# Optimization experiments

Hardware: AMD Instinct MI355X
Metric: run time of the kernel (lower is better)

The kernel has to match this reference:

```python
import jax, jax.numpy as jnp
import numpy as np

B, T, D = 64, 2048, 256
HID, M = 32, 3
EPS = 1e-8


def _xavier(k, shape):
    lim = (6.0 / (shape[0] + shape[1])) ** 0.5
    return jax.random.uniform(k, shape, jnp.float32, -lim, lim)


def setup_inputs() -> dict:
    key = jax.random.key(0)
    ks = jax.random.split(key, 8)
    h = jax.random.normal(ks[0], (B, T, D), dtype=jnp.float32)
    mask = jax.random.randint(ks[1], (B, T, D), 0, 2).astype(jnp.int32)
    return dict(
        h=h, mask=mask,
        Wa1=_xavier(ks[2], (D, HID)), ba1=jnp.zeros((HID,), jnp.float32),
        Wa2=_xavier(ks[3], (HID, 1)), ba2=jnp.zeros((1,), jnp.float32),
        Wr1=_xavier(ks[4], (D, HID)), br1=jnp.zeros((HID,), jnp.float32),
        Wr2=_xavier(ks[5], (HID, HID)), br2=jnp.zeros((HID,), jnp.float32),
        Wr3=_xavier(ks[6], (HID, M)), br3=jnp.zeros((M,), jnp.float32),
        temperature=jnp.ones((1,), jnp.float32),
    )


def _enhanced_stats(x, mask):
    Bn, Tn, Dn = x.shape
    dt = x.dtype
    # --- temporal: lag-1 autocorrelation (uncentered) + linear trend slope ---
    autocorr = jnp.mean(x[:, :-1, :] * x[:, 1:, :], axis=(1, 2))[:, None]
    t = jnp.arange(Tn, dtype=dt)
    tc = t - t.mean()
    xm_t = x.mean(axis=2)  # (B,T)
    num = jnp.sum(tc * (xm_t - xm_t.mean(axis=1, keepdims=True)), axis=1, keepdims=True)
    trend = num / (jnp.sum(tc ** 2) + EPS)
    # --- frequency: dominant freq + spectral entropy of channel-mean signal ---
    power = jnp.abs(jnp.fft.rfft(xm_t, axis=1)) ** 2  # (B, T//2+1)
    dom_freq = (jnp.argmax(power, axis=1).astype(dt) / (Tn / 2))[:, None]
    pn = power / (power.sum(axis=1, keepdims=True) + EPS)
    spec_ent = -jnp.sum(pn * jnp.log(pn + EPS), axis=1, keepdims=True)
    # --- statistical: skew, kurtosis, quantiles over all (T*D) values ---
    xc = x - x.mean(axis=(1, 2), keepdims=True)
    m2 = jnp.mean(xc ** 2, axis=(1, 2))
    m3 = jnp.mean(xc ** 3, axis=(1, 2))
    m4 = jnp.mean(xc ** 4, axis=(1, 2))
    skew = m3 / (m2 ** 1.5 + EPS)
    kurt = m4 / (m2 ** 2 + EPS)
    xf = x.reshape(Bn, -1)
    q = jnp.quantile(xf, jnp.array([0.25, 0.5, 0.75], dtype=dt), axis=1)  # (3,B)
    stat = jnp.stack([skew, kurt, q[0], q[1], q[2]], axis=1)
    # --- shape: peak count, zero crossings, rate of change ---
    diff = xm_t[:, 1:] - xm_t[:, :-1]
    peak = jnp.sum((diff[:, 1:] * diff[:, :-1] < 0).astype(dt), axis=1, keepdims=True) / (Tn - 2)
    xct = xm_t - xm_t.mean(axis=1, keepdims=True)
    zc = jnp.sum((xct[:, 1:] * xct[:, :-1] < 0).astype(dt), axis=1, keepdims=True) / (Tn - 1)
    roc = jnp.mean(jnp.abs(diff), axis=1, keepdims=True)
    # --- missing-data features ---
    mf = mask.astype(dt)
    observed = mf.reshape(Bn, -1).sum(axis=1, keepdims=True)
    miss_rate = 1.0 - observed / (Tn * Dn + EPS)
    dens = mf.sum(axis=2) / (Dn + EPS)  # (B,T)
    dens_var = jnp.var(dens, axis=1, ddof=1, keepdims=True)
    tmask = mf.sum(axis=2) > 0
    first_obs = jnp.where(tmask.any(axis=1, keepdims=True),
                          jnp.argmax(tmask, axis=1, keepdims=True).astype(dt) / Tn, 0.0)
    # --- channel features: mean off-diag corr + PCA top var-explained ---
    xcm = x - x.mean(axis=1, keepdims=True)  # (B,T,D)
    gram = jnp.einsum('btd,bte->bde', xcm, xcm)  # (B,D,D) = Xc^T Xc
    cov = gram / (Tn - 1 + EPS)
    std = jnp.std(x, axis=1, ddof=1)  # (B,D)
    corr = cov / (std[:, :, None] * std[:, None, :] + EPS)
    off_diag = 1.0 - jnp.eye(Dn, dtype=dt)
    mean_corr = (jnp.sum(corr * off_diag, axis=(1, 2)) / (Dn * (Dn - 1) + EPS))[:, None]
    # singular values of Xc squared == eigenvalues of Xc^T Xc
    ev = jnp.linalg.eigvalsh(gram)  # ascending (B,D)
    var_exp = (ev[:, -1] / jnp.sum(ev, axis=1))[:, None]
    return jnp.concatenate([autocorr, trend, dom_freq, spec_ent, stat,
                            peak, zc, roc, miss_rate, dens_var, first_obs,
                            mean_corr, var_exp], axis=1)  # (B, 17)


def _direct_routing(h, Wa1, ba1, Wa2, ba2, Wr1, br1, Wr2, br2, Wr3, br3, temperature):
    attn_logits = jnp.tanh(h @ Wa1 + ba1) @ Wa2 + ba2  # (B,T,1)
    attn_w = jax.nn.softmax(attn_logits, axis=1)
    h_pooled = jnp.sum(h * attn_w, axis=1)  # (B,D)
    z = jax.nn.relu(h_pooled @ Wr1 + br1)   # dropout is identity in eval
    z = jax.nn.relu(z @ Wr2 + br2)
    logits = z @ Wr3 + br3
    temp = jnp.clip(temperature, 0.5, 2.0)
    alpha = jax.nn.softmax(logits / temp, axis=-1)
    return alpha, h_pooled


def reference(h, mask, Wa1, ba1, Wa2, ba2, Wr1, br1, Wr2, br2, Wr3, br3, temperature):
    alpha, h_pooled = _direct_routing(h, Wa1, ba1, Wa2, ba2,
                                      Wr1, br1, Wr2, br2, Wr3, br3, temperature)
    stats = _enhanced_stats(h, mask)
    return alpha, h_pooled, stats
```

## Files before the change

### kernel.cpp

```cpp
#include <hip/hip_runtime.h>
#include <math.h>
#include <stdint.h>

#define B 64
#define T 2048
#define D 256
#define HID 32
#define NSEL 6
#define NBIN 8192
#define CAP 8192
#define LCAP 2048
#define EPS 1e-8

#define A_S1 0
#define A_S2 1
#define A_S3 2
#define A_S4 3
#define A_AC 4
#define A_Y2 5
#define A_DIAG 6
#define A_TRACE 7
#define A_N 16

#define NAPPLY 32

typedef __attribute__((ext_vector_type(4))) short short4v;
typedef __attribute__((ext_vector_type(8))) short short8v;
typedef __attribute__((ext_vector_type(4))) float f32x4;

__device__ __forceinline__ unsigned int f2key(float f) {
    unsigned int u = __float_as_uint(f);
    return (u & 0x80000000u) ? ~u : (u | 0x80000000u);
}
__device__ __forceinline__ float key2f(unsigned int k) {
    unsigned int u = (k & 0x80000000u) ? (k ^ 0x80000000u) : ~k;
    return __uint_as_float(u);
}
__device__ __forceinline__ short f2bf(float f) {
    unsigned int u = __float_as_uint(f);
    unsigned int r = u + 0x7FFFu + ((u >> 16) & 1u);
    return (short)(r >> 16);
}

__global__ __launch_bounds__(256) void k_pass1(const float* __restrict__ x, const int* __restrict__ mask,
        double* __restrict__ xm, float* __restrict__ rowm,
        double* __restrict__ cs1, double* __restrict__ cs2, double* __restrict__ accum) {
    int b = blockIdx.x >> 4;
    int blk = blockIdx.x & 15;
    int wave = threadIdx.x >> 6;
    int lane = threadIdx.x & 63;
    int ts = blk * 128 + wave * 32;
    const float* xb = x + (size_t)b * T * D;
    const int* mb = mask + (size_t)b * T * D;
    double c1l[4] = {0, 0, 0, 0}, c2l[4] = {0, 0, 0, 0};
    double s1 = 0, s2 = 0, s3 = 0, s4 = 0, ac = 0;
    float pa[4] = {0, 0, 0, 0};
    for (int r = 0; r < 32; ++r) {
        int t = ts + r;
        float4 xv = *(const float4*)(xb + (size_t)t * D + lane * 4);
        int4 mv = *(const int4*)(mb + (size_t)t * D + lane * 4);
        double rs = (double)xv.x + (double)xv.y + (double)xv.z + (double)xv.w;
        int rm = mv.x + mv.y + mv.z + mv.w;
        for (int o = 32; o > 0; o >>= 1) { rs += __shfl_down(rs, o); rm += __shfl_down(rm, o); }
        if (lane == 0) {
            xm[(size_t)b * T + t] = rs * (1.0 / 256.0);
            rowm[(size_t)b * T + t] = (float)rm;
        }
        float xa[4] = {xv.x, xv.y, xv.z, xv.w};
        #pragma unroll
        for (int j = 0; j < 4; ++j) {
            double xd = (double)xa[j];
            double x2 = xd * xd;
            s1 += xd; s2 += x2; s3 += x2 * xd; s4 += x2 * x2;
            c1l[j] += xd; c2l[j] += x2;
        }
        if (r > 0) {
            #pragma unroll
            for (int j = 0; j < 4; ++j) ac += (double)pa[j] * (double)xa[j];
        }
        pa[0] = xa[0]; pa[1] = xa[1]; pa[2] = xa[2]; pa[3] = xa[3];
    }
    if (ts + 32 <= T - 1) {
        float4 xn = *(const float4*)(xb + (size_t)(ts + 32) * D + lane * 4);
        float na[4] = {xn.x, xn.y, xn.z, xn.w};
        #pragma unroll
        for (int j = 0; j < 4; ++j) ac += (double)pa[j] * (double)na[j];
    }
    for (int o = 32; o > 0; o >>= 1) {
        s1 += __shfl_down(s1, o); s2 += __shfl_down(s2, o);
        s3 += __shfl_down(s3, o); s4 += __shfl_down(s4, o);
        ac += __shfl_down(ac, o);
    }
    if (lane == 0) {
        atomicAdd(&accum[b * A_N + A_S1], s1);
        atomicAdd(&accum[b * A_N + A_S2], s2);
        atomicAdd(&accum[b * A_N + A_S3], s3);
        atomicAdd(&accum[b * A_N + A_S4], s4);
        atomicAdd(&accum[b * A_N + A_AC], ac);
    }
    #pragma unroll
    for (int j = 0; j < 4; ++j) {
        atomicAdd(&cs1[b * D + lane * 4 + j], c1l[j]);
        atomicAdd(&cs2[b * D + lane * 4 + j], c2l[j]);
    }
}

__global__ __launch_bounds__(256) void k_chan(const double* __restrict__ cs1, const double* __restrict__ cs2,
        float* __restrict__ mu, float* __restrict__ winv, double* __restrict__ accum) {
    int b = blockIdx.x, d = threadIdx.x;
    double c1 = cs1[b * D + d], c2 = cs2[b * D + d];
    double m = c1 / (double)T;
    double c2c = c2 - c1 * c1 / (double)T;
    double var = c2c / (double)(T - 1);
    mu[b * D + d] = (float)m;
    winv[b * D + d] = (float)(1.0 / sqrt(var));
    double diag = (c2c / ((double)(T - 1) + EPS)) / (var + EPS);
    __shared__ double sd[256], st[256];
    sd[d] = diag; st[d] = c2c; __syncthreads();
    for (int o = 128; o > 0; o >>= 1) {
        if (d < o) { sd[d] += sd[d + o]; st[d] += st[d + o]; }
        __syncthreads();
    }
    if (d == 0) { accum[b * A_N + A_DIAG] = sd[0]; accum[b * A_N + A_TRACE] = st[0]; }
}

__global__ __launch_bounds__(256) void k_attn(const float* __restrict__ x,
        const float* __restrict__ Wa1, const float* __restrict__ ba1,
        const float* __restrict__ Wa2, const float* __restrict__ ba2,
        float* __restrict__ logit) {
    __shared__ float tile[256][33];
    int bid = blockIdx.x;
    int b = bid >> 3, t0 = (bid & 7) * 256;
    int tid = threadIdx.x;
    const float* xb = x + (size_t)b * T * D + (size_t)t0 * D;
    float acc[HID];
    #pragma unroll
    for (int h = 0; h < HID; ++h) acc[h] = 0.f;
    for (int dc = 0; dc < 8; ++dc) {
        __syncthreads();
        #pragma unroll
        for (int i = 0; i < 32; ++i) {
            int idx = i * 256 + tid;
            int tl = idx >> 5, dd = idx & 31;
            tile[tl][dd] = xb[(size_t)tl * D + dc * 32 + dd];
        }
        __syncthreads();
        #pragma unroll
        for (int dd = 0; dd < 32; ++dd) {
            float xval = tile[tid][dd];
            const float* wrow = Wa1 + (dc * 32 + dd) * HID;
            #pragma unroll
            for (int h = 0; h < HID; ++h) acc[h] += xval * wrow[h];
        }
    }
    float lg = ba2[0];
    #pragma unroll
    for (int h = 0; h < HID; ++h) lg += tanhf(acc[h] + ba1[h]) * Wa2[h];
    logit[(size_t)b * T + t0 + tid] = lg;
}

__global__ __launch_bounds__(256) void k_smax(const float* __restrict__ logit, float* __restrict__ smz) {
    int b = blockIdx.x, tid = threadIdx.x;
    __shared__ float sm[256];
    __shared__ double sz[256];
    float mx = -1e30f;
    for (int i = tid; i < T; i += 256) mx = fmaxf(mx, logit[(size_t)b * T + i]);
    sm[tid] = mx; __syncthreads();
    for (int o = 128; o > 0; o >>= 1) { if (tid < o) sm[tid] = fmaxf(sm[tid], sm[tid + o]); __syncthreads(); }
    float m = sm[0];
    double z = 0;
    for (int i = tid; i < T; i += 256) z += (double)expf(logit[(size_t)b * T + i] - m);
    sz[tid] = z; __syncthreads();
    for (int o = 128; o > 0; o >>= 1) { if (tid < o) sz[tid] += sz[tid + o]; __syncthreads(); }
    if (tid == 0) { smz[b * 2] = m; smz[b * 2 + 1] = (float)sz[0]; }
}

__global__ __launch_bounds__(256) void k_pool(const float* __restrict__ x,
        const float* __restrict__ logit, const float* __restrict__ smz,
        const float* __restrict__ mu, const float* __restrict__ winv,
        float* __restrict__ hpool, double* __restrict__ accum) {
    int bid = blockIdx.x;
    int b = bid >> 3, t0 = (bid & 7) * 256;
    int wave = threadIdx.x >> 6, lane = threadIdx.x & 63;
    const float* xb = x + (size_t)b * T * D;
    float m = smz[b * 2], Z = smz[b * 2 + 1];
    float4 mu4 = *(const float4*)(mu + b * D + lane * 4);
    float4 w4 = *(const float4*)(winv + b * D + lane * 4);
    double p0 = 0, p1 = 0, p2 = 0, p3 = 0, yacc = 0;
    for (int r = 0; r < 64; ++r) {
        int t = t0 + wave * 64 + r;
        float4 xv = *(const float4*)(xb + (size_t)t * D + lane * 4);
        float wt = expf(logit[(size_t)b * T + t] - m) / Z;
        p0 += (double)(wt * xv.x); p1 += (double)(wt * xv.y);
        p2 += (double)(wt * xv.z); p3 += (double)(wt * xv.w);
        double y = (double)((xv.x - mu4.x) * w4.x) + (double)((xv.y - mu4.y) * w4.y)
                 + (double)((xv.z - mu4.z) * w4.z) + (double)((xv.w - mu4.w) * w4.w);
        for (int o = 32; o > 0; o >>= 1) y += __shfl_down(y, o);
        if (lane == 0) yacc += y * y;
    }
    if (lane == 0) atomicAdd(&accum[b * A_N + A_Y2], yacc);
    atomicAdd(&hpool[b * D + lane * 4 + 0], (float)p0);
    atomicAdd(&hpool[b * D + lane * 4 + 1], (float)p1);
    atomicAdd(&hpool[b * D + lane * 4 + 2], (float)p2);
    atomicAdd(&hpool[b * D + lane * 4 + 3], (float)p3);
}

__global__ void k_route(const float* __restrict__ hpool,
        const float* __restrict__ Wr1, const float* __restrict__ br1,
        const float* __restrict__ Wr2, const float* __restrict__ br2,
        const float* __restrict__ Wr3, const float* __restrict__ br3,
        const float* __restrict__ temperature, float* __restrict__ alpha) {
    int b = blockIdx.x, tid = threadIdx.x;
    __shared__ float z1[HID], z2[HID], hp[D];
    for (int i = tid; i < D; i += 64) hp[i] = hpool[b * D + i];
    __syncthreads();
    if (tid < HID) {
        float a = br1[tid];
        for (int d = 0; d < D; ++d) a += hp[d] * Wr1[d * HID + tid];
        z1[tid] = fmaxf(a, 0.f);
    }
    __syncthreads();
    if (tid < HID) {
        float a = br2[tid];
        for (int j = 0; j < HID; ++j) a += z1[j] * Wr2[j * HID + tid];
        z2[tid] = fmaxf(a, 0.f);
    }
    __syncthreads();
    if (tid == 0) {
        float tmp = temperature[0];
        tmp = fminf(fmaxf(tmp, 0.5f), 2.0f);
        float lg[3];
        for (int k = 0; k < 3; ++k) {
            float a = br3[k];
            for (int j = 0; j < HID; ++j) a += z2[j] * Wr3[j * 3 + k];
            lg[k] = a / tmp;
        }
        float mx = fmaxf(lg[0], fmaxf(lg[1], lg[2]));
        float e0 = expf(lg[0] - mx), e1 = expf(lg[1] - mx), e2 = expf(lg[2] - mx);
        float s = e0 + e1 + e2;
        alpha[b * 3 + 0] = e0 / s; alpha[b * 3 + 1] = e1 / s; alpha[b * 3 + 2] = e2 / s;
    }
}

__global__ __launch_bounds__(256) void k_xmstats(const double* __restrict__ xm,
        const float* __restrict__ rowm, const double* __restrict__ accum,
        float* __restrict__ stats) {
    int b = blockIdx.x, tid = threadIdx.x;
    __shared__ double xs[T];
    __shared__ double r0[256], r1[256], r2[256];
    __shared__ int i0[256], i1[256];
    const double* xmb = xm + (size_t)b * T;
    for (int i = tid; i < T; i += 256) xs[i] = xmb[i];
    __syncthreads();
    double ls = 0;
    for (int i = tid; i < T; i += 256) ls += xs[i];
    r0[tid] = ls; __syncthreads();
    for (int o = 128; o > 0; o >>= 1) { if (tid < o) r0[tid] += r0[tid + o]; __syncthreads(); }
    double xmean = r0[0] / (double)T;
    __syncthreads();
    double tn = 0, roc = 0; int pk = 0, zc = 0;
    for (int i = tid; i < T; i += 256) {
        tn += ((double)i - 1023.5) * (xs[i] - xmean);
        if (i <= T - 2) {
            double d1 = xs[i + 1] - xs[i];
            roc += fabs(d1);
            if (i >= 1) { double d0 = xs[i] - xs[i - 1]; if (d0 * d1 < 0.0) pk++; }
            if ((xs[i] - xmean) * (xs[i + 1] - xmean) < 0.0) zc++;
        }
    }
    r0[tid] = tn; r1[tid] = roc; i0[tid] = pk; i1[tid] = zc; __syncthreads();
    for (int o = 128; o > 0; o >>= 1) {
        if (tid < o) { r0[tid] += r0[tid + o]; r1[tid] += r1[tid + o]; i0[tid] += i0[tid + o]; i1[tid] += i1[tid + o]; }
        __syncthreads();
    }
    double trendnum = r0[0], rocsum = r1[0];
    int pks = i0[0], zcs = i1[0];
    __syncthreads();
    double ds = 0, ds2 = 0, obs = 0; int ft = T;
    for (int i = tid; i < T; i += 256) {
        double rm = (double)rowm[(size_t)b * T + i];
        obs += rm;
        double dn = rm / (256.0 + EPS);
        ds += dn; ds2 += dn * dn;
        if (rm > 0.0 && i < ft) ft = i;
    }
    r0[tid] = ds; r1[tid] = ds2; r2[tid] = obs; i0[tid] = ft; __syncthreads();
    for (int o = 128; o > 0; o >>= 1) {
        if (tid < o) { r0[tid] += r0[tid + o]; r1[tid] += r1[tid + o]; r2[tid] += r2[tid + o]; i0[tid] = min(i0[tid], i0[tid + o]); }
        __syncthreads();
    }
    if (tid == 0) {
        double dsum = r0[0], dsq = r1[0], obst = r2[0]; int ftt = i0[0];
        const double n = (double)T * (double)D;
        const double* ab = accum + b * A_N;
        double s1 = ab[A_S1], s2 = ab[A_S2], s3 = ab[A_S3], s4 = ab[A_S4];
        double acv = ab[A_AC], y2 = ab[A_Y2], dg = ab[A_DIAG];
        double mu_ = s1 / n;
        double m2 = s2 / n - mu_ * mu_;
        double m3 = s3 / n - 3.0 * mu_ * (s2 / n) + 2.0 * mu_ * mu_ * mu_;
        double m4 = s4 / n - 4.0 * mu_ * (s3 / n) + 6.0 * mu_ * mu_ * (s2 / n) - 3.0 * mu_ * mu_ * mu_ * mu_;
        float* st = stats + b * 17;
        st[0] = (float)(acv / ((double)(T - 1) * (double)D));
        st[1] = (float)(trendnum / (715827712.0 + EPS));
        st[4] = (float)(m3 / (sqrt(m2) * m2 + EPS));
        st[5] = (float)(m4 / (m2 * m2 + EPS));
        st[9] = (float)((double)pks / (double)(T - 2));
        st[10] = (float)((double)zcs / (double)(T - 1));
        st[11] = (float)(rocsum / (double)(T - 1));
        st[12] = (float)(1.0 - obst / ((double)T * (double)D + EPS));
        double dmean = dsum / (double)T;
        st[13] = (float)((dsq - dsum * dmean) / (double)(T - 1));
        st[14] = (ftt < T) ? (float)((double)ftt / (double)T) : 0.0f;
        st[15] = (float)((y2 / ((double)(T - 1) + EPS) - dg) / ((double)D * (D - 1) + EPS));
    }
}

__global__ __launch_bounds__(256) void k_dft(const double* __restrict__ xm, double* __restrict__ power) {
    __shared__ double xs[T];
    int b = blockIdx.x / 5, kc = blockIdx.x % 5;
    int tid = threadIdx.x;
    for (int i = tid; i < T; i += 256) xs[i] = xm[(size_t)b * T + i];
    __syncthreads();
    int k = kc * 256 + tid;
    if (k <= T / 2) {
        double theta = -6.283185307179586476925286766559 * (double)k / (double)T;
        double c4 = cos(4.0 * theta), s4 = sin(4.0 * theta);
        double cr = 1.0, ci = 0.0;
        double a0r = 0, a0i = 0, a1r = 0, a1i = 0, a2r = 0, a2i = 0, a3r = 0, a3i = 0;
        #pragma unroll 4
        for (int p = 0; p < T / 4; ++p) {
            double x0 = xs[4 * p + 0], x1 = xs[4 * p + 1];
            double x2 = xs[4 * p + 2], x3 = xs[4 * p + 3];
            a0r += x0 * cr; a0i += x0 * ci;
            a1r += x1 * cr; a1i += x1 * ci;
            a2r += x2 * cr; a2i += x2 * ci;
            a3r += x3 * cr; a3i += x3 * ci;
            double ncr = cr * c4 - ci * s4;
            double nci = cr * s4 + ci * c4;
            cr = ncr; ci = nci;
        }
        double c1 = cos(theta), s1 = sin(theta);
        double ar = a0r, ai = a0i;
        ar += c1 * a1r - s1 * a1i; ai += c1 * a1i + s1 * a1r;
        double c2 = c1 * c1 - s1 * s1, s2 = 2.0 * c1 * s1;
        ar += c2 * a2r - s2 * a2i; ai += c2 * a2i + s2 * a2r;
        double c3 = c2 * c1 - s2 * s1, s3 = c2 * s1 + s2 * c1;
        ar += c3 * a3r - s3 * a3i; ai += c3 * a3i + s3 * a3r;
        power[(size_t)b * 1025 + k] = ar * ar + ai * ai;
    }
}

__global__ __launch_bounds__(256) void k_spec(const double* __restrict__ power, float* __restrict__ stats) {
    int b = blockIdx.x, tid = threadIdx.x;
    __shared__ double rv[256];
    __shared__ int ri[256];
    const double* pb = power + (size_t)b * 1025;
    double bm = -1.0; int bi = 0; double lsum = 0;
    for (int i = tid; i < 1025; i += 256) {
        double p = pb[i];
        lsum += p;
        if (p > bm) { bm = p; bi = i; }
    }
    rv[tid] = bm; ri[tid] = bi; __syncthreads();
    for (int o = 128; o > 0; o >>= 1) {
        if (tid < o) {
            if (rv[tid + o] > rv[tid] || (rv[tid + o] == rv[tid] && ri[tid + o] < ri[tid])) {
                rv[tid] = rv[tid + o]; ri[tid] = ri[tid + o];
            }
        }
        __syncthreads();
    }
    int amax = ri[0];
    __syncthreads();
    rv[tid] = lsum; __syncthreads();
    for (int o = 128; o > 0; o >>= 1) { if (tid < o) rv[tid] += rv[tid + o]; __syncthreads(); }
    double S = rv[0] + EPS;
    __syncthreads();
    double le = 0;
    for (int i = tid; i < 1025; i += 256) {
        double pn = pb[i] / S;
        le -= pn * log(pn + EPS);
    }
    rv[tid] = le; __syncthreads();
    for (int o = 128; o > 0; o >>= 1) { if (tid < o) rv[tid] += rv[tid + o]; __syncthreads(); }
    if (tid == 0) {
        stats[b * 17 + 2] = (float)((double)amax / (double)(T / 2));
        stats[b * 17 + 3] = (float)rv[0];
    }
}

__global__ __launch_bounds__(256) void k_histA(const float* __restrict__ x, unsigned int* __restrict__ hist) {
    __shared__ unsigned int lh[NBIN];
    int b = blockIdx.x >> 2, chunk = blockIdx.x & 3;
    int tid = threadIdx.x;
    for (int i = tid; i < NBIN; i += 256) lh[i] = 0;
    __syncthreads();
    const float4* xb = (const float4*)(x + (size_t)b * T * D + (size_t)chunk * (T * D / 4));
    for (int i = tid; i < T * D / 16; i += 256) {
        float4 v = xb[i];
        atomicAdd(&lh[f2key(v.x) >> 19], 1u);
        atomicAdd(&lh[f2key(v.y) >> 19], 1u);
        atomicAdd(&lh[f2key(v.z) >> 19], 1u);
        atomicAdd(&lh[f2key(v.w) >> 19], 1u);
    }
    __syncthreads();
    for (int i = tid; i < NBIN; i += 256)
        if (lh[i]) atomicAdd(&hist[(size_t)b * NBIN + i], lh[i]);
}

__global__ __launch_bounds__(256) void k_histB(const unsigned int* __restrict__ hist,
        unsigned int* __restrict__ binsel, unsigned int* __restrict__ krem) {
    int b = blockIdx.x, tid = threadIdx.x;
    __shared__ unsigned int seg[256], base[256];
    const unsigned int* hb = hist + (size_t)b * NBIN;
    unsigned int s = 0;
    for (int i = 0; i < 32; ++i) s += hb[tid * 32 + i];
    seg[tid] = s; __syncthreads();
    if (tid == 0) {
        unsigned int run = 0;
        for (int i = 0; i < 256; ++i) { base[i] = run; run += seg[i]; }
    }
    __syncthreads();
    const unsigned int targets[NSEL] = {131071u, 131072u, 262143u, 262144u, 393215u, 393216u};
    for (int q = 0; q < NSEL; ++q) {
        unsigned int k = targets[q];
        if (k >= base[tid] && k < base[tid] + seg[tid]) {
            unsigned int run = base[tid];
            for (int i = 0; i < 32; ++i) {
                unsigned int c = hb[tid * 32 + i];
                if (k < run + c) { binsel[b * NSEL + q] = tid * 32 + i; krem[b * NSEL + q] = k - run; break; }
                run += c;
            }
        }
    }
}

__global__ __launch_bounds__(256) void k_compact(const float* __restrict__ x,
        const unsigned int* __restrict__ binsel, unsigned int* __restrict__ ccnt,
        unsigned int* __restrict__ cand) {
    __shared__ unsigned int lbuf[NSEL][LCAP];
    __shared__ unsigned int lcnt[NSEL];
    __shared__ unsigned int gbase[NSEL];
    int b = blockIdx.x >> 4, chunk = blockIdx.x & 15;
    int tid = threadIdx.x;
    if (tid < NSEL) lcnt[tid] = 0;
    unsigned int bs[NSEL];
    #pragma unroll
    for (int q = 0; q < NSEL; ++q) bs[q] = binsel[b * NSEL + q];
    __syncthreads();
    const float4* xb = (const float4*)(x + (size_t)b * T * D + (size_t)chunk * (T * D / 16));
    for (int it = 0; it < 32; ++it) {
        float4 v = xb[it * 256 + tid];
        float va[4] = {v.x, v.y, v.z, v.w};
        #pragma unroll
        for (int j = 0; j < 4; ++j) {
            unsigned int u = f2key(va[j]);
            unsigned int bin = u >> 19;
            #pragma unroll
            for (int q = 0; q < NSEL; ++q) {
                if (bin == bs[q]) {
                    unsigned int p = atomicAdd(&lcnt[q], 1u);
                    if (p < LCAP) lbuf[q][p] = u;
                }
            }
        }
        __syncthreads();
        bool need = false;
        #pragma unroll
        for (int q = 0; q < NSEL; ++q) need = need || (lcnt[q] > (unsigned)(LCAP - 1024));
        if (need) {
            if (tid < NSEL) {
                unsigned int n = min(lcnt[tid], (unsigned)LCAP);
                gbase[tid] = atomicAdd(&ccnt[b * NSEL + tid], n);
            }
            __syncthreads();
            #pragma unroll
            for (int q = 0; q < NSEL; ++q) {
                unsigned int n = min(lcnt[q], (unsigned)LCAP);
                unsigned int g0 = gbase[q];
                for (unsigned int i = tid; i < n; i += 256) {
                    unsigned int p = g0 + i;
                    if (p < CAP) cand[((size_t)b * NSEL + q) * CAP + p] = lbuf[q][i];
                }
            }
            __syncthreads();
            if (tid < NSEL) lcnt[tid] = 0;
            __syncthreads();
        }
    }
    __syncthreads();
    if (tid < NSEL) {
        unsigned int n = min(lcnt[tid], (unsigned)LCAP);
        gbase[tid] = atomicAdd(&ccnt[b * NSEL + tid], n);
    }
    __syncthreads();
    #pragma unroll
    for (int q = 0; q < NSEL; ++q) {
        unsigned int n = min(lcnt[q], (unsigned)LCAP);
        unsigned int g0 = gbase[q];
        for (unsigned int i = tid; i < n; i += 256) {
            unsigned int p = g0 + i;
            if (p < CAP) cand[((size_t)b * NSEL + q) * CAP + p] = lbuf[q][i];
        }
    }
}

__global__ __launch_bounds__(256) void k_select(const unsigned int* __restrict__ cand,
        const unsigned int* __restrict__ ccnt, const unsigned int* __restrict__ binsel,
        const unsigned int* __restrict__ krem, float* __restrict__ qv) {
    int b = blockIdx.x / NSEL, q = blockIdx.x % NSEL;
    int tid = threadIdx.x;
    __shared__ unsigned int lc[CAP];
    __shared__ unsigned int rc[256];
    unsigned int n = ccnt[b * NSEL + q];
    if (n > CAP) n = CAP;
    for (unsigned int i = tid; i < n; i += 256) lc[i] = cand[((size_t)b * NSEL + q) * CAP + i];
    __syncthreads();
    unsigned int prefix = binsel[b * NSEL + q] << 19;
    unsigned int k = krem[b * NSEL + q];
    for (int bit = 18; bit >= 0; --bit) {
        unsigned int hi = prefix >> (bit + 1);
        unsigned int c = 0;
        for (unsigned int i = tid; i < n; i += 256) {
            unsigned int u = lc[i];
            if ((u >> (bit + 1)) == hi && !((u >> bit) & 1u)) c++;
        }
        rc[tid] = c; __syncthreads();
        for (int o = 128; o > 0; o >>= 1) { if (tid < o) rc[tid] += rc[tid + o]; __syncthreads(); }
        unsigned int c0 = rc[0];
        __syncthreads();
        if (k >= c0) { k -= c0; prefix |= (1u << bit); }
    }
    if (tid == 0) qv[b * NSEL + q] = key2f(prefix);
}

__global__ void k_qwrite(const float* __restrict__ qv, float* __restrict__ stats) {
    int b = threadIdx.x;
    if (b >= B) return;
    const float* qq = qv + b * NSEL;
    double q25 = 0.25 * (double)qq[0] + 0.75 * (double)qq[1];
    double q50 = 0.5 * ((double)qq[2] + (double)qq[3]);
    double q75 = 0.75 * (double)qq[4] + 0.25 * (double)qq[5];
    stats[b * 17 + 6] = (float)q25;
    stats[b * 17 + 7] = (float)q50;
    stats[b * 17 + 8] = (float)q75;
}

#define GROWS 72
__global__ __launch_bounds__(256) void k_gram(const float* __restrict__ x, const float* __restrict__ mu,
        float* __restrict__ gram) {
    __shared__ __align__(16) short lds_a[128 * GROWS];
    __shared__ __align__(16) short lds_b[128 * GROWS];
    int b = blockIdx.x >> 2;
    int ti = (blockIdx.x >> 1) & 1, tj = blockIdx.x & 1;
    int i0 = ti * 128, j0 = tj * 128;
    int tid = threadIdx.x;
    int w = tid >> 6, lane = tid & 63;
    int qd = lane >> 4, l15 = lane & 15;
    const float* xb = x + (size_t)b * T * D;
    const float* mub = mu + (size_t)b * D;
    int mc = tid & 31;
    float4 mua = *(const float4*)(mub + i0 + 4 * mc);
    float4 mub4 = *(const float4*)(mub + j0 + 4 * mc);
    f32x4 acc[2][8];
    #pragma unroll
    for (int rt = 0; rt < 2; ++rt)
        #pragma unroll
        for (int ct = 0; ct < 8; ++ct) acc[rt][ct] = (f32x4){0.f, 0.f, 0.f, 0.f};
    for (int t0 = 0; t0 < T; t0 += 64) {
        __syncthreads();
        #pragma unroll
        for (int half = 0; half < 2; ++half) {
            int mtt = (tid >> 5) + half * 8;
            int t = t0 + 4 * mtt;
            int tblk = mtt >> 1;
            int sub = (mtt & 1) * 4;
            int rot = (tblk + mc) & 7;
            {
                const float* src = xb + (size_t)t * D + i0 + 4 * mc;
                float4 r0 = *(const float4*)(src);
                float4 r1 = *(const float4*)(src + D);
                float4 r2 = *(const float4*)(src + 2 * D);
                float4 r3 = *(const float4*)(src + 3 * D);
                float a0[4] = {r0.x - mua.x, r0.y - mua.y, r0.z - mua.z, r0.w - mua.w};
                float a1[4] = {r1.x - mua.x, r1.y - mua.y, r1.z - mua.z, r1.w - mua.w};
                float a2[4] = {r2.x - mua.x, r2.y - mua.y, r2.z - mua.z, r2.w - mua.w};
                float a3[4] = {r3.x - mua.x, r3.y - mua.y, r3.z - mua.z, r3.w - mua.w};
                #pragma unroll
                for (int j = 0; j < 4; ++j) {
                    int c = 4 * mc + j;
                    short4v v4 = {f2bf(a0[j]), f2bf(a1[j]), f2bf(a2[j]), f2bf(a3[j])};
                    *(short4v*)(lds_a + c * GROWS + rot * 8 + sub) = v4;
                }
            }
            {
                const float* src = xb + (size_t)t * D + j0 + 4 * mc;
                float4 r0 = *(const float4*)(src);
                float4 r1 = *(const float4*)(src + D);
                float4 r2 = *(const float4*)(src + 2 * D);
                float4 r3 = *(const float4*)(src + 3 * D);
                float a0[4] = {r0.x - mub4.x, r0.y - mub4.y, r0.z - mub4.z, r0.w - mub4.w};
                float a1[4] = {r1.x - mub4.x, r1.y - mub4.y, r1.z - mub4.z, r1.w - mub4.w};
                float a2[4] = {r2.x - mub4.x, r2.y - mub4.y, r2.z - mub4.z, r2.w - mub4.w};
                float a3[4] = {r3.x - mub4.x, r3.y - mub4.y, r3.z - mub4.z, r3.w - mub4.w};
                #pragma unroll
                for (int j = 0; j < 4; ++j) {
                    int c = 4 * mc + j;
                    short4v v4 = {f2bf(a0[j]), f2bf(a1[j]), f2bf(a2[j]), f2bf(a3[j])};
                    *(short4v*)(lds_b + c * GROWS + rot * 8 + sub) = v4;
                }
            }
        }
        __syncthreads();
        #pragma unroll
        for (int kc = 0; kc < 2; ++kc) {
            int tblk = kc * 4 + qd;
            short8v af[2];
            #pragma unroll
            for (int rt = 0; rt < 2; ++rt) {
                int c = w * 32 + rt * 16 + l15;
                int rot = (tblk + (c >> 2)) & 7;
                af[rt] = *(const short8v*)(lds_a + c * GROWS + rot * 8);
            }
            short8v bfr[8];
            #pragma unroll
            for (int ct = 0; ct < 8; ++ct) {
                int c = ct * 16 + l15;
                int rot = (tblk + (c >> 2)) & 7;
                bfr[ct] = *(const short8v*)(lds_b + c * GROWS + rot * 8);
            }
            #pragma unroll
            for (int rt = 0; rt < 2; ++rt)
                #pragma unroll
                for (int ct = 0; ct < 8; ++ct)
                    acc[rt][ct] = __builtin_amdgcn_mfma_f32_16x16x32_bf16(af[rt], bfr[ct], acc[rt][ct], 0, 0, 0);
        }
    }
    float* gb = gram + (size_t)b * D * D;
    #pragma unroll
    for (int rt = 0; rt < 2; ++rt) {
        int rbase = i0 + w * 32 + rt * 16 + qd * 4;
        #pragma unroll
        for (int ct = 0; ct < 8; ++ct) {
            int cc = j0 + ct * 16 + l15;
            #pragma unroll
            for (int reg = 0; reg < 4; ++reg)
                gb[(size_t)(rbase + reg) * D + cc] = acc[rt][ct][reg];
        }
    }
}

__global__ __launch_bounds__(1024) void k_power(const float* __restrict__ gram,
        const double* __restrict__ accum, float* __restrict__ stats) {
    int b = blockIdx.x;
    int tid = threadIdx.x;
    int row = tid & 255, sl = tid >> 8;
    __shared__ __align__(16) float v[2][D];
    __shared__ float part[1024];
    __shared__ double dpart[1024];
    const float* g = gram + (size_t)b * D * D + (size_t)row * D + sl * 64;
    float gr[64];
    #pragma unroll
    for (int j = 0; j < 64; j += 4) {
        float4 t4 = *(const float4*)(g + j);
        gr[j] = t4.x; gr[j + 1] = t4.y; gr[j + 2] = t4.z; gr[j + 3] = t4.w;
    }
    if (tid < D) {
        float h = sinf((float)tid * 12.9898f) * 43758.547f;
        v[0][tid] = h - floorf(h) - 0.4375f;
    }
    __syncthreads();
    int cur = 0;
    for (int it = 0; it < NAPPLY; ++it) {
        const float* vv = &v[cur][sl * 64];
        float acc = 0.f;
        #pragma unroll
        for (int j = 0; j < 64; j += 4) {
            float4 vb = *(const float4*)(vv + j);
            acc += gr[j] * vb.x + gr[j + 1] * vb.y + gr[j + 2] * vb.z + gr[j + 3] * vb.w;
        }
        part[tid] = acc; __syncthreads();
        if (tid < D) v[cur ^ 1][tid] = part[tid] + part[tid + 256] + part[tid + 512] + part[tid + 768];
        cur ^= 1;
        if ((it & 7) == 7 || it == NAPPLY - 1) {
            __syncthreads();
            double nl = 0;
            if (tid < D) { double yv = (double)v[cur][tid]; nl = yv * yv; }
            dpart[tid] = nl; __syncthreads();
            for (int o = 512; o > 0; o >>= 1) { if (tid < o) dpart[tid] += dpart[tid + o]; __syncthreads(); }
            float inv = (float)(1.0 / sqrt(dpart[0]));
            __syncthreads();
            if (tid < D) v[cur][tid] *= inv;
        }
        __syncthreads();
    }
    const float* vv = &v[cur][sl * 64];
    float acc = 0.f;
    #pragma unroll
    for (int j = 0; j < 64; j += 4) {
        float4 vb = *(const float4*)(vv + j);
        acc += gr[j] * vb.x + gr[j + 1] * vb.y + gr[j + 2] * vb.z + gr[j + 3] * vb.w;
    }
    part[tid] = acc; __syncthreads();
    double num = 0, den = 0;
    if (tid < D) {
        double wv = (double)part[tid] + (double)part[tid + 256] + (double)part[tid + 512] + (double)part[tid + 768];
        double vd = (double)v[cur][tid];
        num = vd * wv; den = vd * vd;
    }
    dpart[tid] = num; __syncthreads();
    for (int o = 512; o > 0; o >>= 1) { if (tid < o) dpart[tid] += dpart[tid + o]; __syncthreads(); }
    double lam = dpart[0];
    __syncthreads();
    dpart[tid] = den; __syncthreads();
    for (int o = 512; o > 0; o >>= 1) { if (tid < o) dpart[tid] += dpart[tid + o]; __syncthreads(); }
    if (tid == 0) {
        double trace = accum[b * A_N + A_TRACE];
        stats[b * 17 + 16] = (float)(lam / dpart[0] / trace);
    }
}

extern "C" void kernel_launch(void* const* d_in, const int* in_sizes, int n_in,
                              void* d_out, int out_size, void* d_ws, size_t ws_size,
                              hipStream_t stream) {
    (void)in_sizes; (void)n_in; (void)ws_size;
    const float* x    = (const float*)d_in[0];
    const int*   mask = (const int*)d_in[1];
    const float* Wa1  = (const float*)d_in[2];
    const float* ba1  = (const float*)d_in[3];
    const float* Wa2  = (const float*)d_in[4];
    const float* ba2  = (const float*)d_in[5];
    const float* Wr1  = (const float*)d_in[6];
    const float* br1  = (const float*)d_in[7];
    const float* Wr2  = (const float*)d_in[8];
    const float* br2  = (const float*)d_in[9];
    const float* Wr3  = (const float*)d_in[10];
    const float* br3  = (const float*)d_in[11];
    const float* temp = (const float*)d_in[12];

    float* out = (float*)d_out;
    float* alpha = out;
    float* hpool = out + 192;
    float* stats = out + 192 + 16384;

    char* w = (char*)d_ws;
    size_t off = 0;
    auto alloc = [&](size_t bytes) -> char* {
        char* p = w + off;
        off = (off + bytes + 255) & ~(size_t)255;
        return p;
    };
    double* cs1 = (double*)alloc((size_t)B * D * 8);
    double* cs2 = (double*)alloc((size_t)B * D * 8);
    double* accum = (double*)alloc((size_t)B * A_N * 8);
    unsigned int* ccnt = (unsigned int*)alloc((size_t)B * NSEL * 4);
    unsigned int* hist = (unsigned int*)alloc((size_t)B * NBIN * 4);
    size_t zero_bytes = off;
    double* xm = (double*)alloc((size_t)B * T * 8);
    float* rowm = (float*)alloc((size_t)B * T * 4);
    float* logit = (float*)alloc((size_t)B * T * 4);
    float* smz = (float*)alloc((size_t)B * 2 * 4);
    float* mu = (float*)alloc((size_t)B * D * 4);
    float* winv = (float*)alloc((size_t)B * D * 4);
    double* power = (double*)alloc((size_t)B * 1025 * 8);
    unsigned int* binsel = (unsigned int*)alloc((size_t)B * NSEL * 4);
    unsigned int* krem = (unsigned int*)alloc((size_t)B * NSEL * 4);
    float* qv = (float*)alloc((size_t)B * NSEL * 4);
    size_t union_bytes = (size_t)B * D * D * 4;
    char* ureg = alloc(union_bytes);
    unsigned int* cand = (unsigned int*)ureg;
    float* gram = (float*)ureg;

    hipMemsetAsync(d_ws, 0, zero_bytes, stream);
    hipMemsetAsync(d_out, 0, (size_t)out_size * 4, stream);

    k_pass1<<<B * 16, 256, 0, stream>>>(x, mask, xm, rowm, cs1, cs2, accum);
    k_chan<<<B, 256, 0, stream>>>(cs1, cs2, mu, winv, accum);
    k_attn<<<B * 8, 256, 0, stream>>>(x, Wa1, ba1, Wa2, ba2, logit);
    k_smax<<<B, 256, 0, stream>>>(logit, smz);
    k_pool<<<B * 8, 256, 0, stream>>>(x, logit, smz, mu, winv, hpool, accum);
    k_route<<<B, 64, 0, stream>>>(hpool, Wr1, br1, Wr2, br2, Wr3, br3, temp, alpha);
    k_xmstats<<<B, 256, 0, stream>>>(xm, rowm, accum, stats);
    k_dft<<<B * 5, 256, 0, stream>>>(xm, power);
    k_spec<<<B, 256, 0, stream>>>(power, stats);
    k_histA<<<B * 4, 256, 0, stream>>>(x, hist);
    k_histB<<<B, 256, 0, stream>>>(hist, binsel, krem);
    k_compact<<<B * 16, 256, 0, stream>>>(x, binsel, ccnt, cand);
    k_select<<<B * NSEL, 256, 0, stream>>>(cand, ccnt, binsel, krem, qv);
    k_qwrite<<<1, 64, 0, stream>>>(qv, stats);
    k_gram<<<B * 4, 256, 0, stream>>>(x, mu, gram);
    k_power<<<B, 1024, 0, stream>>>(gram, accum, stats);
}
```

Baseline: 865.2 us.

## Replace per-row shuffles and global atomics with LDS partial reductions

In k_pass1 and k_pool, the full-wave double-precision shuffle reductions per row are replaced by 4-lane float partial sums staged in shared memory and reduced after the loop. The per-channel global atomicAdds become per-block partial buffers, which k_chan and k_route sum. k_route is widened to 256 threads and now writes hpool itself. This cuts shuffle latency and atomic contention. In exchange, row sums and pooled accumulation run in float instead of double, which may shift precision slightly.

```diff
diff --git a/kernel.cpp b/kernel.cpp
--- a/kernel.cpp
+++ b/kernel.cpp
@@ -42,13 +42,19 @@
     return (short)(r >> 16);
 }
 
+#define RST 132
 __global__ __launch_bounds__(256) void k_pass1(const float* __restrict__ x, const int* __restrict__ mask,
         double* __restrict__ xm, float* __restrict__ rowm,
-        double* __restrict__ cs1, double* __restrict__ cs2, double* __restrict__ accum) {
+        double* __restrict__ cs1p, double* __restrict__ cs2p, double* __restrict__ accum) {
+    __shared__ float rsb[16 * RST];
+    __shared__ float rmb[16 * RST];
+    __shared__ double cbuf[4][64][8];
+    __shared__ double sacc[4][5];
     int b = blockIdx.x >> 4;
     int blk = blockIdx.x & 15;
     int wave = threadIdx.x >> 6;
     int lane = threadIdx.x & 63;
+    int tid = threadIdx.x;
     int ts = blk * 128 + wave * 32;
     const float* xb = x + (size_t)b * T * D;
     const int* mb = mask + (size_t)b * T * D;
@@ -59,12 +65,14 @@
         int t = ts + r;
         float4 xv = *(const float4*)(xb + (size_t)t * D + lane * 4);
         int4 mv = *(const int4*)(mb + (size_t)t * D + lane * 4);
-        double rs = (double)xv.x + (double)xv.y + (double)xv.z + (double)xv.w;
-        int rm = mv.x + mv.y + mv.z + mv.w;
-        for (int o = 32; o > 0; o >>= 1) { rs += __shfl_down(rs, o); rm += __shfl_down(rm, o); }
-        if (lane == 0) {
-            xm[(size_t)b * T + t] = rs * (1.0 / 256.0);
-            rowm[(size_t)b * T + t] = (float)rm;
+        float rsf = xv.x + xv.y + xv.z + xv.w;
+        float rmf = (float)(mv.x + mv.y + mv.z + mv.w);
+        rsf += __shfl_xor(rsf, 1); rsf += __shfl_xor(rsf, 2);
+        rmf += __shfl_xor(rmf, 1); rmf += __shfl_xor(rmf, 2);
+        int q = wave * 32 + r;
+        if ((lane & 3) == 0) {
+            rsb[(lane >> 2) * RST + q] = rsf;
+            rmb[(lane >> 2) * RST + q] = rmf;
         }
         float xa[4] = {xv.x, xv.y, xv.z, xv.w};
         #pragma unroll
@@ -92,23 +100,46 @@
         ac += __shfl_down(ac, o);
     }
     if (lane == 0) {
-        atomicAdd(&accum[b * A_N + A_S1], s1);
-        atomicAdd(&accum[b * A_N + A_S2], s2);
-        atomicAdd(&accum[b * A_N + A_S3], s3);
-        atomicAdd(&accum[b * A_N + A_S4], s4);
-        atomicAdd(&accum[b * A_N + A_AC], ac);
+        sacc[wave][0] = s1; sacc[wave][1] = s2; sacc[wave][2] = s3;
+        sacc[wave][3] = s4; sacc[wave][4] = ac;
     }
     #pragma unroll
     for (int j = 0; j < 4; ++j) {
-        atomicAdd(&cs1[b * D + lane * 4 + j], c1l[j]);
-        atomicAdd(&cs2[b * D + lane * 4 + j], c2l[j]);
-    }
-}
-
-__global__ __launch_bounds__(256) void k_chan(const double* __restrict__ cs1, const double* __restrict__ cs2,
+        cbuf[wave][lane][j] = c1l[j];
+        cbuf[wave][lane][4 + j] = c2l[j];
+    }
+    __syncthreads();
+    if (tid < 128) {
+        float rs = 0.f, rm = 0.f;
+        #pragma unroll
+        for (int k = 0; k < 16; ++k) { rs += rsb[k * RST + tid]; rm += rmb[k * RST + tid]; }
+        xm[(size_t)b * T + blk * 128 + tid] = (double)rs * (1.0 / 256.0);
+        rowm[(size_t)b * T + blk * 128 + tid] = rm;
+    }
+    if (tid < 64) {
+        #pragma unroll
+        for (int j = 0; j < 4; ++j) {
+            double c1 = cbuf[0][tid][j] + cbuf[1][tid][j] + cbuf[2][tid][j] + cbuf[3][tid][j];
+            double c2 = cbuf[0][tid][4 + j] + cbuf[1][tid][4 + j] + cbuf[2][tid][4 + j] + cbuf[3][tid][4 + j];
+            cs1p[((size_t)b * 16 + blk) * 256 + tid * 4 + j] = c1;
+            cs2p[((size_t)b * 16 + blk) * 256 + tid * 4 + j] = c2;
+        }
+    }
+    if (tid < 5) {
+        double s = sacc[0][tid] + sacc[1][tid] + sacc[2][tid] + sacc[3][tid];
+        atomicAdd(&accum[b * A_N + tid], s);
+    }
+}
+
+__global__ __launch_bounds__(256) void k_chan(const double* __restrict__ cs1p, const double* __restrict__ cs2p,
         float* __restrict__ mu, float* __restrict__ winv, double* __restrict__ accum) {
     int b = blockIdx.x, d = threadIdx.x;
-    double c1 = cs1[b * D + d], c2 = cs2[b * D + d];
+    double c1 = 0, c2 = 0;
+    #pragma unroll
+    for (int k = 0; k < 16; ++k) {
+        c1 += cs1p[((size_t)b * 16 + k) * 256 + d];
+        c2 += cs2p[((size_t)b * 16 + k) * 256 + d];
+    }
     double m = c1 / (double)T;
     double c2c = c2 - c1 * c1 / (double)T;
     double var = c2c / (double)(T - 1);
@@ -175,44 +206,70 @@
     if (tid == 0) { smz[b * 2] = m; smz[b * 2 + 1] = (float)sz[0]; }
 }
 
+#define YST 260
 __global__ __launch_bounds__(256) void k_pool(const float* __restrict__ x,
         const float* __restrict__ logit, const float* __restrict__ smz,
         const float* __restrict__ mu, const float* __restrict__ winv,
-        float* __restrict__ hpool, double* __restrict__ accum) {
+        float* __restrict__ hpoolp, double* __restrict__ accum) {
+    __shared__ float ybuf[16 * YST];
+    __shared__ float pbuf[4][64][4];
+    __shared__ double dred[256];
     int bid = blockIdx.x;
-    int b = bid >> 3, t0 = (bid & 7) * 256;
+    int b = bid >> 3, blk = bid & 7, t0 = blk * 256;
     int wave = threadIdx.x >> 6, lane = threadIdx.x & 63;
+    int tid = threadIdx.x;
     const float* xb = x + (size_t)b * T * D;
     float m = smz[b * 2], Z = smz[b * 2 + 1];
     float4 mu4 = *(const float4*)(mu + b * D + lane * 4);
     float4 w4 = *(const float4*)(winv + b * D + lane * 4);
-    double p0 = 0, p1 = 0, p2 = 0, p3 = 0, yacc = 0;
+    float p0 = 0.f, p1 = 0.f, p2 = 0.f, p3 = 0.f;
     for (int r = 0; r < 64; ++r) {
         int t = t0 + wave * 64 + r;
         float4 xv = *(const float4*)(xb + (size_t)t * D + lane * 4);
         float wt = expf(logit[(size_t)b * T + t] - m) / Z;
-        p0 += (double)(wt * xv.x); p1 += (double)(wt * xv.y);
-        p2 += (double)(wt * xv.z); p3 += (double)(wt * xv.w);
-        double y = (double)((xv.x - mu4.x) * w4.x) + (double)((xv.y - mu4.y) * w4.y)
-                 + (double)((xv.z - mu4.z) * w4.z) + (double)((xv.w - mu4.w) * w4.w);
-        for (int o = 32; o > 0; o >>= 1) y += __shfl_down(y, o);
-        if (lane == 0) yacc += y * y;
-    }
-    if (lane == 0) atomicAdd(&accum[b * A_N + A_Y2], yacc);
-    atomicAdd(&hpool[b * D + lane * 4 + 0], (float)p0);
-    atomicAdd(&hpool[b * D + lane * 4 + 1], (float)p1);
-    atomicAdd(&hpool[b * D + lane * 4 + 2], (float)p2);
-    atomicAdd(&hpool[b * D + lane * 4 + 3], (float)p3);
-}
-
-__global__ void k_route(const float* __restrict__ hpool,
+        p0 += wt * xv.x; p1 += wt * xv.y; p2 += wt * xv.z; p3 += wt * xv.w;
+        float yl = (xv.x - mu4.x) * w4.x + (xv.y - mu4.y) * w4.y
+                 + (xv.z - mu4.z) * w4.z + (xv.w - mu4.w) * w4.w;
+        yl += __shfl_xor(yl, 1); yl += __shfl_xor(yl, 2);
+        int q = wave * 64 + r;
+        if ((lane & 3) == 0) ybuf[(lane >> 2) * YST + q] = yl;
+    }
+    pbuf[wave][lane][0] = p0; pbuf[wave][lane][1] = p1;
+    pbuf[wave][lane][2] = p2; pbuf[wave][lane][3] = p3;
+    __syncthreads();
+    {
+        float y = 0.f;
+        #pragma unroll
+        for (int k = 0; k < 16; ++k) y += ybuf[k * YST + tid];
+        dred[tid] = (double)y * (double)y;
+    }
+    __syncthreads();
+    for (int o = 128; o > 0; o >>= 1) { if (tid < o) dred[tid] += dred[tid + o]; __syncthreads(); }
+    if (tid == 0) atomicAdd(&accum[b * A_N + A_Y2], dred[0]);
+    if (tid < 64) {
+        #pragma unroll
+        for (int j = 0; j < 4; ++j) {
+            float s = pbuf[0][tid][j] + pbuf[1][tid][j] + pbuf[2][tid][j] + pbuf[3][tid][j];
+            hpoolp[((size_t)b * 8 + blk) * 256 + tid * 4 + j] = s;
+        }
+    }
+}
+
+__global__ __launch_bounds__(256) void k_route(const float* __restrict__ hpoolp,
         const float* __restrict__ Wr1, const float* __restrict__ br1,
         const float* __restrict__ Wr2, const float* __restrict__ br2,
         const float* __restrict__ Wr3, const float* __restrict__ br3,
-        const float* __restrict__ temperature, float* __restrict__ alpha) {
+        const float* __restrict__ temperature, float* __restrict__ hpool,
+        float* __restrict__ alpha) {
     int b = blockIdx.x, tid = threadIdx.x;
     __shared__ float z1[HID], z2[HID], hp[D];
-    for (int i = tid; i < D; i += 64) hp[i] = hpool[b * D + i];
+    {
+        float s = 0.f;
+        #pragma unroll
+        for (int k = 0; k < 8; ++k) s += hpoolp[((size_t)b * 8 + k) * 256 + tid];
+        hp[tid] = s;
+        hpool[b * D + tid] = s;
+    }
     __syncthreads();
     if (tid < HID) {
         float a = br1[tid];
@@ -750,8 +807,6 @@
         off = (off + bytes + 255) & ~(size_t)255;
         return p;
     };
-    double* cs1 = (double*)alloc((size_t)B * D * 8);
-    double* cs2 = (double*)alloc((size_t)B * D * 8);
     double* accum = (double*)alloc((size_t)B * A_N * 8);
     unsigned int* ccnt = (unsigned int*)alloc((size_t)B * NSEL * 4);
     unsigned int* hist = (unsigned int*)alloc((size_t)B * NBIN * 4);
@@ -768,18 +823,21 @@
     float* qv = (float*)alloc((size_t)B * NSEL * 4);
     size_t union_bytes = (size_t)B * D * D * 4;
     char* ureg = alloc(union_bytes);
+    double* cs1p = (double*)ureg;
+    double* cs2p = (double*)(ureg + (size_t)B * 16 * 256 * 8);
+    float* hpoolp = (float*)(ureg + 2 * (size_t)B * 16 * 256 * 8);
     unsigned int* cand = (unsigned int*)ureg;
     float* gram = (float*)ureg;
 
     hipMemsetAsync(d_ws, 0, zero_bytes, stream);
     hipMemsetAsync(d_out, 0, (size_t)out_size * 4, stream);
 
-    k_pass1<<<B * 16, 256, 0, stream>>>(x, mask, xm, rowm, cs1, cs2, accum);
-    k_chan<<<B, 256, 0, stream>>>(cs1, cs2, mu, winv, accum);
+    k_pass1<<<B * 16, 256, 0, stream>>>(x, mask, xm, rowm, cs1p, cs2p, accum);
+    k_chan<<<B, 256, 0, stream>>>(cs1p, cs2p, mu, winv, accum);
     k_attn<<<B * 8, 256, 0, stream>>>(x, Wa1, ba1, Wa2, ba2, logit);
     k_smax<<<B, 256, 0, stream>>>(logit, smz);
-    k_pool<<<B * 8, 256, 0, stream>>>(x, logit, smz, mu, winv, hpool, accum);
-    k_route<<<B, 64, 0, stream>>>(hpool, Wr1, br1, Wr2, br2, Wr3, br3, temp, alpha);
+    k_pool<<<B * 8, 256, 0, stream>>>(x, logit, smz, mu, winv, hpoolp, accum);
+    k_route<<<B, 256, 0, stream>>>(hpoolp, Wr1, br1, Wr2, br2, Wr3, br3, temp, hpool, alpha);
     k_xmstats<<<B, 256, 0, stream>>>(xm, rowm, accum, stats);
     k_dft<<<B * 5, 256, 0, stream>>>(xm, power);
     k_spec<<<B, 256, 0, stream>>>(power, stats);
```

Result: faster. 816.2 us (-5.7%).
